# Performance work log

Hardware: AMD Instinct MI355X
Metric: run time of the kernel (lower is better)

## Reference

```python
import jax, jax.numpy as jnp
import numpy as np

EMBED_DIM = 1024
LATEN_DIM = 1024
B, S = 4, 2048


def setup_inputs() -> dict:
    key = jax.random.key(0)
    k1, k2, k3, k4, k5 = jax.random.split(key, 5)
    xq = jax.random.normal(k1, (B, S, EMBED_DIM), dtype=jnp.float32)
    xk = jax.random.normal(k2, (B, S, EMBED_DIM), dtype=jnp.float32)
    xv = jax.random.normal(k3, (B, S, EMBED_DIM), dtype=jnp.float32)
    # Linear weight init similar to torch default scale
    bound = 1.0 / np.sqrt(EMBED_DIM)
    Wq = jax.random.uniform(k4, (EMBED_DIM, EMBED_DIM), minval=-bound, maxval=bound, dtype=jnp.float32)
    bq = jax.random.uniform(k5, (EMBED_DIM,), minval=-bound, maxval=bound, dtype=jnp.float32)
    # causal mask: 1 => masked (future positions)
    att_mask = jnp.triu(jnp.ones((S, S), dtype=jnp.int32), k=1)
    return {"xq": xq, "xk": xk, "xv": xv, "Wq": Wq, "bq": bq, "att_mask": att_mask}


def reference(xq, xk, xv, Wq, bq, att_mask):
    scale = LATEN_DIM ** (-0.5)
    # Faithful to source: linearQ is applied to all three inputs.
    Q = jnp.einsum('bsd,ed->bse', xq, Wq) + bq
    K = jnp.einsum('bsd,ed->bse', xk, Wq) + bq
    V = jnp.einsum('bsd,ed->bse', xv, Wq) + bq
    scores = jnp.einsum('bqe,bke->bqk', Q, K) * scale  # [B, S, S]
    scores = jnp.where(att_mask == 1, -jnp.inf, scores)
    probs = jax.nn.softmax(scores, axis=-1)
    return jnp.einsum('bqk,bke->bqe', probs, V)
```

## Files before the change

kernel.cpp:

```cpp
#include <hip/hip_runtime.h>
#include <hip/hip_bf16.h>
#include <stdint.h>


typedef __attribute__((ext_vector_type(8))) short bf16x8;
typedef __attribute__((ext_vector_type(4))) float floatx4;

#define DEVI static __device__ __forceinline__

static constexpr int S_ = 2048;
static constexpr int E_ = 1024;
static constexpr int BATCH = 4;
static constexpr int N4X = 8192 * 1024 / 4;

DEVI unsigned short f2b(float f) {
  union { float f; unsigned u; } v; v.f = f;
  return (unsigned short)((v.u + 0x7FFFu + ((v.u >> 16) & 1u)) >> 16);
}

DEVI void async_load16(const void* g, void* l) {
  __builtin_amdgcn_global_load_lds(
      (__attribute__((address_space(1))) void*)(void*)(g),
      (__attribute__((address_space(3))) void*)(l),
      16, 0, 0);
}


DEVI void stage64(const unsigned short* __restrict__ src, unsigned short* ls,
                  int ld, int tid) {
#pragma unroll
  for (int j = 0; j < 4; ++j) {
    const int u = tid + j * 256;
    const int row = u >> 3, slot = u & 7;
    async_load16(src + (size_t)row * ld + ((slot ^ (row & 7)) << 3),
                 ls + u * 8);
  }
}

DEVI bf16x8 ldfrag64(const unsigned short* ls, int r, int c) {
  return *(const bf16x8*)(ls + r * 64 + ((c ^ (r & 7)) << 3));
}

DEVI void mfma_tile64(const unsigned short* lsA, const unsigned short* lsB,
                      int m0, int n0, int lrow, int g, floatx4 (&acc)[4][4]) {
#pragma unroll
  for (int ks = 0; ks < 2; ++ks) {
    bf16x8 af[4], bfr[4];
#pragma unroll
    for (int i = 0; i < 4; ++i)
      af[i] = ldfrag64(lsA, m0 + i * 16 + lrow, ks * 4 + g);
#pragma unroll
    for (int i = 0; i < 4; ++i)
      bfr[i] = ldfrag64(lsB, n0 + i * 16 + lrow, ks * 4 + g);
#pragma unroll
    for (int mi = 0; mi < 4; ++mi)
#pragma unroll
      for (int ni = 0; ni < 4; ++ni)
        acc[mi][ni] = __builtin_amdgcn_mfma_f32_16x16x32_bf16(
            af[mi], bfr[ni], acc[mi][ni], 0, 0, 0);
  }
}

__global__ void cvt_all(const float* __restrict__ xq,
                        const float* __restrict__ xk,
                        const float* __restrict__ xv,
                        const float* __restrict__ Wq,
                        unsigned short* __restrict__ Xb,
                        unsigned short* __restrict__ Wb) {
  int i = blockIdx.x * blockDim.x + threadIdx.x;
  const float4* src;
  ushort4* dst;
  if (i < 3 * N4X) {
    int seg = i / N4X, off = i - seg * N4X;
    const float* s = (seg == 0) ? xq : (seg == 1) ? xk : xv;
    src = (const float4*)s + off;
    dst = (ushort4*)(Xb + (size_t)seg * 8192 * 1024) + off;
  } else {
    int off = i - 3 * N4X;
    src = (const float4*)Wq + off;
    dst = (ushort4*)Wb + off;
  }
  float4 v = *src;
  ushort4 o;
  o.x = f2b(v.x); o.y = f2b(v.y); o.z = f2b(v.z); o.w = f2b(v.w);
  *dst = o;
}

__global__ __launch_bounds__(256) void gemm_qkv(
    const unsigned short* __restrict__ Xb, const unsigned short* __restrict__ Wb,
    const float* __restrict__ bias, unsigned short* __restrict__ Qb,
    unsigned short* __restrict__ Kb, unsigned short* __restrict__ Vt) {
  __shared__ __align__(16) unsigned short lsA[128 * 64];
  __shared__ __align__(16) unsigned short lsB[128 * 64];
  const int l = blockIdx.x;
  const int xcd = l & 7, i = l >> 3;
  const int bn = i & 7;
  const int bmg = xcd * 24 + (i >> 3);
  const int input = bmg / 64, bm = bmg % 64;
  const unsigned short* A = Xb + (size_t)bmg * 128 * 1024;
  const unsigned short* W = Wb + (size_t)bn * 128 * 1024;

  const int tid = threadIdx.x;
  const int lane = tid & 63, wave = tid >> 6;
  const int m0 = (wave >> 1) * 64, n0 = (wave & 1) * 64;
  const int lrow = lane & 15, g = lane >> 4;

  floatx4 acc[4][4] = {};
  for (int kt = 0; kt < 16; ++kt) {
    if (kt) __syncthreads();
    stage64(A + kt * 64, lsA, 1024, tid);
    stage64(W + kt * 64, lsB, 1024, tid);
    __syncthreads();
    mfma_tile64(lsA, lsB, m0, n0, lrow, g, acc);
  }

  unsigned short* C = (input == 0) ? Qb : (input == 1) ? Kb : Vt;
  const int rb = (lane >> 4) * 4;
#pragma unroll
  for (int mi = 0; mi < 4; ++mi)
#pragma unroll
    for (int ni = 0; ni < 4; ++ni) {
      int gcol = bn * 128 + n0 + ni * 16 + lrow;
      float bv = bias[gcol];
#pragma unroll
      for (int r = 0; r < 4; ++r) {
        int grow = bm * 128 + m0 + mi * 16 + rb + r;
        unsigned short val = f2b(acc[mi][ni][r] + bv);
        if (input == 2) {
          int b = grow >> 11, s = grow & 2047;
          C[((size_t)b * 1024 + gcol) * 2048 + s] = val;
        } else {
          C[(size_t)grow * 1024 + gcol] = val;
        }
      }
    }
}

__global__ __launch_bounds__(256) void gemm_scores_exp(
    const unsigned short* __restrict__ Qb,
    const unsigned short* __restrict__ Kb, unsigned short* __restrict__ P,
    float* __restrict__ lsum) {
  const int l = blockIdx.x;
  const int xcd = l & 7, k = l >> 3;
  const int m = k & 7, gl = k >> 3;
  const int gg = xcd * 12 + gl;
  const int z = gg / 24, r0 = gg % 24;
  const int bm = (r0 < 8) ? r0 : 8 + ((r0 - 8) >> 1);
  const int bn = ((r0 < 8) ? 0 : ((r0 - 8) & 1)) * 8 + m;
  if (bn > bm) return;

  __shared__ __align__(16) unsigned short lsA[128 * 64];
  __shared__ __align__(16) unsigned short lsB[128 * 64];
  const unsigned short* A = Qb + ((size_t)z * S_ + bm * 128) * E_;
  const unsigned short* Bt = Kb + ((size_t)z * S_ + bn * 128) * E_;
  const int tid = threadIdx.x;
  const int lane = tid & 63, wave = tid >> 6;
  const int m0 = (wave >> 1) * 64, n0 = (wave & 1) * 64;
  const int lrow = lane & 15, g = lane >> 4;

  floatx4 acc[4][4] = {};
  for (int kt = 0; kt < 16; ++kt) {
    if (kt) __syncthreads();
    stage64(A + kt * 64, lsA, E_, tid);
    stage64(Bt + kt * 64, lsB, E_, tid);
    __syncthreads();
    mfma_tile64(lsA, lsB, m0, n0, lrow, g, acc);
  }

  const int rb = (lane >> 4) * 4;
  const bool diag = (bm == bn);
#pragma unroll
  for (int mi = 0; mi < 4; ++mi)
#pragma unroll
    for (int r = 0; r < 4; ++r) {
      const int grow = bm * 128 + m0 + mi * 16 + rb + r;
      float rsum = 0.f;
#pragma unroll
      for (int ni = 0; ni < 4; ++ni) {
        const int gcol = bn * 128 + n0 + ni * 16 + lrow;
        float p = __expf(acc[mi][ni][r] * 0.03125f);
        if (diag && gcol > grow) p = 0.f;
        P[((size_t)z * S_ + grow) * S_ + gcol] = f2b(p);
        rsum += p;
      }
#pragma unroll
      for (int off = 1; off < 16; off <<= 1) rsum += __shfl_xor(rsum, off);
      if ((lane & 15) == 0) atomicAdd(&lsum[z * S_ + grow], rsum);
    }
}

__global__ __launch_bounds__(256) void gemm_pv(
    const unsigned short* __restrict__ Pb,
    const unsigned short* __restrict__ Vt, const float* __restrict__ lsum,
    float* __restrict__ Out) {
  __shared__ __align__(16) unsigned short lsA[128 * 64];
  __shared__ __align__(16) unsigned short lsB[128 * 64];
  const int l = blockIdx.x;
  const int xcd = l & 7, i = l >> 3;
  const int bn = i & 7, j = i >> 3;
  const int z = j >> 1;
  const int bm = (j & 1) ? xcd : 15 - xcd;

  const unsigned short* A = Pb + ((size_t)z * S_ + bm * 128) * S_;
  const unsigned short* Bt = Vt + ((size_t)z * E_ + bn * 128) * S_;
  float* C = Out + (size_t)z * S_ * E_;
  const int tid = threadIdx.x;
  const int lane = tid & 63, wave = tid >> 6;
  const int m0 = (wave >> 1) * 64, n0 = (wave & 1) * 64;
  const int lrow = lane & 15, g = lane >> 4;

  floatx4 acc[4][4] = {};
  const int nKK = (bm + 1) * 2;
  for (int kt = 0; kt < nKK; ++kt) {
    if (kt) __syncthreads();
    stage64(A + kt * 64, lsA, S_, tid);
    stage64(Bt + kt * 64, lsB, S_, tid);
    __syncthreads();
    mfma_tile64(lsA, lsB, m0, n0, lrow, g, acc);
  }

  const int rb = (lane >> 4) * 4;
#pragma unroll
  for (int mi = 0; mi < 4; ++mi)
#pragma unroll
    for (int r = 0; r < 4; ++r) {
      const int grow = bm * 128 + m0 + mi * 16 + rb + r;
      const float inv = 1.0f / lsum[z * S_ + grow];
#pragma unroll
      for (int ni = 0; ni < 4; ++ni) {
        const int gcol = bn * 128 + n0 + ni * 16 + lrow;
        C[(size_t)grow * E_ + gcol] = acc[mi][ni][r] * inv;
      }
    }
}

extern "C" void kernel_launch(void* const* d_in, const int* in_sizes, int n_in,
                              void* d_out, int out_size, void* d_ws,
                              size_t ws_size, hipStream_t stream) {
  (void)in_sizes; (void)n_in; (void)out_size; (void)ws_size;
  const float* xq = (const float*)d_in[0];
  const float* xk = (const float*)d_in[1];
  const float* xv = (const float*)d_in[2];
  const float* Wq = (const float*)d_in[3];
  const float* bq = (const float*)d_in[4];
  float* out = (float*)d_out;

  unsigned short* base16 = (unsigned short*)d_ws;
  unsigned short* Xb = base16;
  unsigned short* P = base16;
  unsigned short* Wb = base16 + (size_t)24 * 1024 * 1024;
  unsigned short* Qb = Wb + (size_t)1024 * 1024;
  unsigned short* Kb = Qb + (size_t)8192 * 1024;
  unsigned short* Vt = Kb + (size_t)8192 * 1024;
  float* lsum = (float*)(Vt + (size_t)8192 * 1024);

  hipMemsetAsync(lsum, 0, BATCH * S_ * sizeof(float), stream);

  const int n4tot = 3 * N4X + 1024 * 1024 / 4;
  cvt_all<<<n4tot / 256, 256, 0, stream>>>(xq, xk, xv, Wq, Xb, Wb);

  gemm_qkv<<<1536, 256, 0, stream>>>(Xb, Wb, bq, Qb, Kb, Vt);
  gemm_scores_exp<<<768, 256, 0, stream>>>(Qb, Kb, P, lsum);
  gemm_pv<<<512, 256, 0, stream>>>(P, Vt, lsum, out);
}
```

Before: 306.0 us.

## Use 64x128 tiles with 128-thread blocks for scores and PV GEMMs

The scores and PV kernels switch from 128x128 tiles on 256 threads to 64x128 tiles on 128 threads (two waves). The scores grid is rebuilt to enumerate only the causal lower-triangle tiles (1088 blocks, none exiting early), and PV uses 1024 blocks with a finer per-row-tile K range. This is meant to cut the masked work wasted above the diagonal and improve load balance across CUs. The cost is lower data reuse per tile, which means more global loads per FLOP.

```diff
diff --git a/kernel.cpp b/kernel.cpp
--- a/kernel.cpp
+++ b/kernel.cpp
@@ -26,11 +26,12 @@
 }
 
 
+template <int ROWS, int NTHR>
 DEVI void stage64(const unsigned short* __restrict__ src, unsigned short* ls,
                   int ld, int tid) {
 #pragma unroll
-  for (int j = 0; j < 4; ++j) {
-    const int u = tid + j * 256;
+  for (int j = 0; j < ROWS * 8 / NTHR; ++j) {
+    const int u = tid + j * NTHR;
     const int row = u >> 3, slot = u & 7;
     async_load16(src + (size_t)row * ld + ((slot ^ (row & 7)) << 3),
                  ls + u * 8);
@@ -108,8 +109,8 @@
   floatx4 acc[4][4] = {};
   for (int kt = 0; kt < 16; ++kt) {
     if (kt) __syncthreads();
-    stage64(A + kt * 64, lsA, 1024, tid);
-    stage64(W + kt * 64, lsB, 1024, tid);
+    stage64<128, 256>(A + kt * 64, lsA, 1024, tid);
+    stage64<128, 256>(W + kt * 64, lsB, 1024, tid);
     __syncthreads();
     mfma_tile64(lsA, lsB, m0, n0, lrow, g, acc);
   }
@@ -136,49 +137,48 @@
     }
 }
 
-__global__ __launch_bounds__(256) void gemm_scores_exp(
+__global__ __launch_bounds__(128) void gemm_scores_exp(
     const unsigned short* __restrict__ Qb,
     const unsigned short* __restrict__ Kb, unsigned short* __restrict__ P,
     float* __restrict__ lsum) {
+  __shared__ __align__(16) unsigned short lsA[64 * 64];
+  __shared__ __align__(16) unsigned short lsB[128 * 64];
   const int l = blockIdx.x;
-  const int xcd = l & 7, k = l >> 3;
-  const int m = k & 7, gl = k >> 3;
-  const int gg = xcd * 12 + gl;
-  const int z = gg / 24, r0 = gg % 24;
-  const int bm = (r0 < 8) ? r0 : 8 + ((r0 - 8) >> 1);
-  const int bn = ((r0 < 8) ? 0 : ((r0 - 8) & 1)) * 8 + m;
-  if (bn > bm) return;
-
-  __shared__ __align__(16) unsigned short lsA[128 * 64];
-  __shared__ __align__(16) unsigned short lsB[128 * 64];
-  const unsigned short* A = Qb + ((size_t)z * S_ + bm * 128) * E_;
-  const unsigned short* Bt = Kb + ((size_t)z * S_ + bn * 128) * E_;
+  const int gid = (l & 7) * 136 + (l >> 3);
+  const int z = gid >> 8 >= 0 ? gid / 272 : 0;
+  int r = gid % 272;
+  int rm = 0;
+  for (;;) { const int c = (rm >> 1) + 1; if (r < c) break; r -= c; ++rm; }
+  const int cn = r;
+
+  const unsigned short* A = Qb + ((size_t)z * S_ + rm * 64) * E_;
+  const unsigned short* Bt = Kb + ((size_t)z * S_ + cn * 128) * E_;
   const int tid = threadIdx.x;
   const int lane = tid & 63, wave = tid >> 6;
-  const int m0 = (wave >> 1) * 64, n0 = (wave & 1) * 64;
+  const int n0 = wave * 64;
   const int lrow = lane & 15, g = lane >> 4;
 
   floatx4 acc[4][4] = {};
   for (int kt = 0; kt < 16; ++kt) {
     if (kt) __syncthreads();
-    stage64(A + kt * 64, lsA, E_, tid);
-    stage64(Bt + kt * 64, lsB, E_, tid);
+    stage64<64, 128>(A + kt * 64, lsA, E_, tid);
+    stage64<128, 128>(Bt + kt * 64, lsB, E_, tid);
     __syncthreads();
-    mfma_tile64(lsA, lsB, m0, n0, lrow, g, acc);
+    mfma_tile64(lsA, lsB, 0, n0, lrow, g, acc);
   }
 
   const int rb = (lane >> 4) * 4;
-  const bool diag = (bm == bn);
+  const bool diag = (cn == (rm >> 1));
 #pragma unroll
   for (int mi = 0; mi < 4; ++mi)
 #pragma unroll
-    for (int r = 0; r < 4; ++r) {
-      const int grow = bm * 128 + m0 + mi * 16 + rb + r;
+    for (int r2 = 0; r2 < 4; ++r2) {
+      const int grow = rm * 64 + mi * 16 + rb + r2;
       float rsum = 0.f;
 #pragma unroll
       for (int ni = 0; ni < 4; ++ni) {
-        const int gcol = bn * 128 + n0 + ni * 16 + lrow;
-        float p = __expf(acc[mi][ni][r] * 0.03125f);
+        const int gcol = cn * 128 + n0 + ni * 16 + lrow;
+        float p = __expf(acc[mi][ni][r2] * 0.03125f);
         if (diag && gcol > grow) p = 0.f;
         P[((size_t)z * S_ + grow) * S_ + gcol] = f2b(p);
         rsum += p;
@@ -189,47 +189,47 @@
     }
 }
 
-__global__ __launch_bounds__(256) void gemm_pv(
+__global__ __launch_bounds__(128) void gemm_pv(
     const unsigned short* __restrict__ Pb,
     const unsigned short* __restrict__ Vt, const float* __restrict__ lsum,
     float* __restrict__ Out) {
-  __shared__ __align__(16) unsigned short lsA[128 * 64];
+  __shared__ __align__(16) unsigned short lsA[64 * 64];
   __shared__ __align__(16) unsigned short lsB[128 * 64];
   const int l = blockIdx.x;
   const int xcd = l & 7, i = l >> 3;
-  const int bn = i & 7, j = i >> 3;
-  const int z = j >> 1;
-  const int bm = (j & 1) ? xcd : 15 - xcd;
-
-  const unsigned short* A = Pb + ((size_t)z * S_ + bm * 128) * S_;
+  const int z = i >> 5, bn = (i >> 2) & 7, s = i & 3;
+  const int pm = (s & 1) ? xcd : 15 - xcd;
+  const int rm = 2 * pm + (s >> 1);
+
+  const unsigned short* A = Pb + ((size_t)z * S_ + rm * 64) * S_;
   const unsigned short* Bt = Vt + ((size_t)z * E_ + bn * 128) * S_;
   float* C = Out + (size_t)z * S_ * E_;
   const int tid = threadIdx.x;
   const int lane = tid & 63, wave = tid >> 6;
-  const int m0 = (wave >> 1) * 64, n0 = (wave & 1) * 64;
+  const int n0 = wave * 64;
   const int lrow = lane & 15, g = lane >> 4;
 
   floatx4 acc[4][4] = {};
-  const int nKK = (bm + 1) * 2;
-  for (int kt = 0; kt < nKK; ++kt) {
+  const int NT = ((rm >> 1) + 1) * 2;
+  for (int kt = 0; kt < NT; ++kt) {
     if (kt) __syncthreads();
-    stage64(A + kt * 64, lsA, S_, tid);
-    stage64(Bt + kt * 64, lsB, S_, tid);
+    stage64<64, 128>(A + kt * 64, lsA, S_, tid);
+    stage64<128, 128>(Bt + kt * 64, lsB, S_, tid);
     __syncthreads();
-    mfma_tile64(lsA, lsB, m0, n0, lrow, g, acc);
+    mfma_tile64(lsA, lsB, 0, n0, lrow, g, acc);
   }
 
   const int rb = (lane >> 4) * 4;
 #pragma unroll
   for (int mi = 0; mi < 4; ++mi)
 #pragma unroll
-    for (int r = 0; r < 4; ++r) {
-      const int grow = bm * 128 + m0 + mi * 16 + rb + r;
+    for (int r2 = 0; r2 < 4; ++r2) {
+      const int grow = rm * 64 + mi * 16 + rb + r2;
       const float inv = 1.0f / lsum[z * S_ + grow];
 #pragma unroll
       for (int ni = 0; ni < 4; ++ni) {
         const int gcol = bn * 128 + n0 + ni * 16 + lrow;
-        C[(size_t)grow * E_ + gcol] = acc[mi][ni][r] * inv;
+        C[(size_t)grow * E_ + gcol] = acc[mi][ni][r2] * inv;
       }
     }
 }
@@ -260,6 +260,6 @@
   cvt_all<<<n4tot / 256, 256, 0, stream>>>(xq, xk, xv, Wq, Xb, Wb);
 
   gemm_qkv<<<1536, 256, 0, stream>>>(Xb, Wb, bq, Qb, Kb, Vt);
-  gemm_scores_exp<<<768, 256, 0, stream>>>(Qb, Kb, P, lsum);
-  gemm_pv<<<512, 256, 0, stream>>>(P, Vt, lsum, out);
-}
+  gemm_scores_exp<<<1088, 128, 0, stream>>>(Qb, Kb, P, lsum);
+  gemm_pv<<<1024, 128, 0, stream>>>(P, Vt, lsum, out);
+}
```

New measurement: 311.1 us. Within noise of the previous version (+1.6%).

## Load attention GEMM fragments directly from global memory, bypassing LDS staging

Applied to the files above, without the earlier changes.

The scores and PV GEMMs stop staging tiles through LDS with barriers. Each wave now loads its MFMA fragments straight from global memory (relying on L2/cache) using a register double-buffered loop. This removes the LDS round trip and the __syncthreads, but each block re-reads data other waves also need and issues less coalesced global loads. The projection GEMM keeps LDS staging with a templated stage function.

```diff
diff --git a/kernel.cpp b/kernel.cpp
--- a/kernel.cpp
+++ b/kernel.cpp
@@ -26,11 +26,12 @@
 }
 
 
+template <int ROWS, int NTHR>
 DEVI void stage64(const unsigned short* __restrict__ src, unsigned short* ls,
                   int ld, int tid) {
 #pragma unroll
-  for (int j = 0; j < 4; ++j) {
-    const int u = tid + j * 256;
+  for (int j = 0; j < ROWS * 8 / NTHR; ++j) {
+    const int u = tid + j * NTHR;
     const int row = u >> 3, slot = u & 7;
     async_load16(src + (size_t)row * ld + ((slot ^ (row & 7)) << 3),
                  ls + u * 8);
@@ -58,6 +59,59 @@
       for (int ni = 0; ni < 4; ++ni)
         acc[mi][ni] = __builtin_amdgcn_mfma_f32_16x16x32_bf16(
             af[mi], bfr[ni], acc[mi][ni], 0, 0, 0);
+  }
+}
+
+
+DEVI void ld_frags(const unsigned short* (&pa)[4], const unsigned short* (&pb)[4],
+                   bf16x8 (&x0)[4], bf16x8 (&x1)[4], bf16x8 (&y0)[4],
+                   bf16x8 (&y1)[4]) {
+#pragma unroll
+  for (int i = 0; i < 4; ++i) {
+    x0[i] = *(const bf16x8*)(pa[i]);
+    x1[i] = *(const bf16x8*)(pa[i] + 32);
+    y0[i] = *(const bf16x8*)(pb[i]);
+    y1[i] = *(const bf16x8*)(pb[i] + 32);
+    pa[i] += 64;
+    pb[i] += 64;
+  }
+}
+
+DEVI void mfma32(const bf16x8 (&x0)[4], const bf16x8 (&x1)[4],
+                 const bf16x8 (&y0)[4], const bf16x8 (&y1)[4],
+                 floatx4 (&acc)[4][4]) {
+#pragma unroll
+  for (int mi = 0; mi < 4; ++mi)
+#pragma unroll
+    for (int ni = 0; ni < 4; ++ni)
+      acc[mi][ni] = __builtin_amdgcn_mfma_f32_16x16x32_bf16(
+          x0[mi], y0[ni], acc[mi][ni], 0, 0, 0);
+#pragma unroll
+  for (int mi = 0; mi < 4; ++mi)
+#pragma unroll
+    for (int ni = 0; ni < 4; ++ni)
+      acc[mi][ni] = __builtin_amdgcn_mfma_f32_16x16x32_bf16(
+          x1[mi], y1[ni], acc[mi][ni], 0, 0, 0);
+}
+
+DEVI void kloop_l2(const unsigned short* __restrict__ A, int lda,
+                   const unsigned short* __restrict__ Bt, int ldb, int NT,
+                   int m0, int n0, int lane, floatx4 (&acc)[4][4]) {
+  const int lrow = lane & 15, g = lane >> 4;
+  const unsigned short* pa[4];
+  const unsigned short* pb[4];
+#pragma unroll
+  for (int i = 0; i < 4; ++i) {
+    pa[i] = A + (size_t)(m0 + i * 16 + lrow) * lda + g * 8;
+    pb[i] = Bt + (size_t)(n0 + i * 16 + lrow) * ldb + g * 8;
+  }
+  bf16x8 a0[4], a1[4], b0[4], b1[4], c0[4], c1[4], d0[4], d1[4];
+  ld_frags(pa, pb, a0, a1, b0, b1);
+  for (int kt = 0; kt + 2 <= NT; kt += 2) {
+    ld_frags(pa, pb, c0, c1, d0, d1);
+    mfma32(a0, a1, b0, b1, acc);
+    if (kt + 2 < NT) ld_frags(pa, pb, a0, a1, b0, b1);
+    mfma32(c0, c1, d0, d1, acc);
   }
 }
 
@@ -108,8 +162,8 @@
   floatx4 acc[4][4] = {};
   for (int kt = 0; kt < 16; ++kt) {
     if (kt) __syncthreads();
-    stage64(A + kt * 64, lsA, 1024, tid);
-    stage64(W + kt * 64, lsB, 1024, tid);
+    stage64<128, 256>(A + kt * 64, lsA, 1024, tid);
+    stage64<128, 256>(W + kt * 64, lsB, 1024, tid);
     __syncthreads();
     mfma_tile64(lsA, lsB, m0, n0, lrow, g, acc);
   }
@@ -149,24 +203,16 @@
   const int bn = ((r0 < 8) ? 0 : ((r0 - 8) & 1)) * 8 + m;
   if (bn > bm) return;
 
-  __shared__ __align__(16) unsigned short lsA[128 * 64];
-  __shared__ __align__(16) unsigned short lsB[128 * 64];
   const unsigned short* A = Qb + ((size_t)z * S_ + bm * 128) * E_;
   const unsigned short* Bt = Kb + ((size_t)z * S_ + bn * 128) * E_;
   const int tid = threadIdx.x;
   const int lane = tid & 63, wave = tid >> 6;
   const int m0 = (wave >> 1) * 64, n0 = (wave & 1) * 64;
-  const int lrow = lane & 15, g = lane >> 4;
 
   floatx4 acc[4][4] = {};
-  for (int kt = 0; kt < 16; ++kt) {
-    if (kt) __syncthreads();
-    stage64(A + kt * 64, lsA, E_, tid);
-    stage64(Bt + kt * 64, lsB, E_, tid);
-    __syncthreads();
-    mfma_tile64(lsA, lsB, m0, n0, lrow, g, acc);
-  }
-
+  kloop_l2(A, E_, Bt, E_, 16, m0, n0, lane, acc);
+
+  const int lrow = lane & 15;
   const int rb = (lane >> 4) * 4;
   const bool diag = (bm == bn);
 #pragma unroll
@@ -193,8 +239,6 @@
     const unsigned short* __restrict__ Pb,
     const unsigned short* __restrict__ Vt, const float* __restrict__ lsum,
     float* __restrict__ Out) {
-  __shared__ __align__(16) unsigned short lsA[128 * 64];
-  __shared__ __align__(16) unsigned short lsB[128 * 64];
   const int l = blockIdx.x;
   const int xcd = l & 7, i = l >> 3;
   const int bn = i & 7, j = i >> 3;
@@ -207,18 +251,12 @@
   const int tid = threadIdx.x;
   const int lane = tid & 63, wave = tid >> 6;
   const int m0 = (wave >> 1) * 64, n0 = (wave & 1) * 64;
-  const int lrow = lane & 15, g = lane >> 4;
 
   floatx4 acc[4][4] = {};
-  const int nKK = (bm + 1) * 2;
-  for (int kt = 0; kt < nKK; ++kt) {
-    if (kt) __syncthreads();
-    stage64(A + kt * 64, lsA, S_, tid);
-    stage64(Bt + kt * 64, lsB, S_, tid);
-    __syncthreads();
-    mfma_tile64(lsA, lsB, m0, n0, lrow, g, acc);
-  }
-
+  const int NT = (bm + 1) * 2;
+  kloop_l2(A, S_, Bt, S_, NT, m0, n0, lane, acc);
+
+  const int lrow = lane & 15;
   const int rb = (lane >> 4) * 4;
 #pragma unroll
   for (int mi = 0; mi < 4; ++mi)
```

Result: slower. 433.2 us (+41.6%).

## Move V projection into scores kernel to fill idle tile slots

Applied to the files above, without the earlier changes.

The V projection GEMM is split out of the QKV kernel and appended as extra blocks (indices 768 and up) of the scores/exp kernel. The Q/K projection kernel now launches only 1024 blocks. The scores grid has many causally-skipped tiles that return immediately, so the V tiles can fill that spare capacity and run alongside the scores work instead of in their own stage. In exchange the fused kernel carries two code paths, and the V-transposed stores may compete with the P writes for memory bandwidth. stage64 is also templated on rows and thread count, with the same values used everywhere.

```diff
diff --git a/kernel.cpp b/kernel.cpp
--- a/kernel.cpp
+++ b/kernel.cpp
@@ -26,11 +26,12 @@
 }
 
 
+template <int ROWS, int NTHR>
 DEVI void stage64(const unsigned short* __restrict__ src, unsigned short* ls,
                   int ld, int tid) {
 #pragma unroll
-  for (int j = 0; j < 4; ++j) {
-    const int u = tid + j * 256;
+  for (int j = 0; j < ROWS * 8 / NTHR; ++j) {
+    const int u = tid + j * NTHR;
     const int row = u >> 3, slot = u & 7;
     async_load16(src + (size_t)row * ld + ((slot ^ (row & 7)) << 3),
                  ls + u * 8);
@@ -86,17 +87,17 @@
   *dst = o;
 }
 
-__global__ __launch_bounds__(256) void gemm_qkv(
+__global__ __launch_bounds__(256) void gemm_qk(
     const unsigned short* __restrict__ Xb, const unsigned short* __restrict__ Wb,
     const float* __restrict__ bias, unsigned short* __restrict__ Qb,
-    unsigned short* __restrict__ Kb, unsigned short* __restrict__ Vt) {
+    unsigned short* __restrict__ Kb) {
   __shared__ __align__(16) unsigned short lsA[128 * 64];
   __shared__ __align__(16) unsigned short lsB[128 * 64];
   const int l = blockIdx.x;
   const int xcd = l & 7, i = l >> 3;
   const int bn = i & 7;
-  const int bmg = xcd * 24 + (i >> 3);
-  const int input = bmg / 64, bm = bmg % 64;
+  const int bmg = xcd * 16 + (i >> 3);
+  const int input = bmg >> 6, bm = bmg & 63;
   const unsigned short* A = Xb + (size_t)bmg * 128 * 1024;
   const unsigned short* W = Wb + (size_t)bn * 128 * 1024;
 
@@ -108,13 +109,13 @@
   floatx4 acc[4][4] = {};
   for (int kt = 0; kt < 16; ++kt) {
     if (kt) __syncthreads();
-    stage64(A + kt * 64, lsA, 1024, tid);
-    stage64(W + kt * 64, lsB, 1024, tid);
+    stage64<128, 256>(A + kt * 64, lsA, 1024, tid);
+    stage64<128, 256>(W + kt * 64, lsB, 1024, tid);
     __syncthreads();
     mfma_tile64(lsA, lsB, m0, n0, lrow, g, acc);
   }
 
-  unsigned short* C = (input == 0) ? Qb : (input == 1) ? Kb : Vt;
+  unsigned short* C = input ? Kb : Qb;
   const int rb = (lane >> 4) * 4;
 #pragma unroll
   for (int mi = 0; mi < 4; ++mi)
@@ -125,68 +126,97 @@
 #pragma unroll
       for (int r = 0; r < 4; ++r) {
         int grow = bm * 128 + m0 + mi * 16 + rb + r;
-        unsigned short val = f2b(acc[mi][ni][r] + bv);
-        if (input == 2) {
-          int b = grow >> 11, s = grow & 2047;
-          C[((size_t)b * 1024 + gcol) * 2048 + s] = val;
-        } else {
-          C[(size_t)grow * 1024 + gcol] = val;
-        }
-      }
-    }
-}
-
-__global__ __launch_bounds__(256) void gemm_scores_exp(
+        C[(size_t)grow * 1024 + gcol] = f2b(acc[mi][ni][r] + bv);
+      }
+    }
+}
+
+__global__ __launch_bounds__(256) void gemm_scores_v(
+    const unsigned short* __restrict__ Xb,
+    const unsigned short* __restrict__ Wb, const float* __restrict__ bias,
     const unsigned short* __restrict__ Qb,
     const unsigned short* __restrict__ Kb, unsigned short* __restrict__ P,
-    float* __restrict__ lsum) {
-  const int l = blockIdx.x;
-  const int xcd = l & 7, k = l >> 3;
-  const int m = k & 7, gl = k >> 3;
-  const int gg = xcd * 12 + gl;
-  const int z = gg / 24, r0 = gg % 24;
-  const int bm = (r0 < 8) ? r0 : 8 + ((r0 - 8) >> 1);
-  const int bn = ((r0 < 8) ? 0 : ((r0 - 8) & 1)) * 8 + m;
-  if (bn > bm) return;
-
+    float* __restrict__ lsum, unsigned short* __restrict__ Vt) {
   __shared__ __align__(16) unsigned short lsA[128 * 64];
   __shared__ __align__(16) unsigned short lsB[128 * 64];
-  const unsigned short* A = Qb + ((size_t)z * S_ + bm * 128) * E_;
-  const unsigned short* Bt = Kb + ((size_t)z * S_ + bn * 128) * E_;
+  const int l = blockIdx.x;
   const int tid = threadIdx.x;
   const int lane = tid & 63, wave = tid >> 6;
   const int m0 = (wave >> 1) * 64, n0 = (wave & 1) * 64;
   const int lrow = lane & 15, g = lane >> 4;
-
-  floatx4 acc[4][4] = {};
-  for (int kt = 0; kt < 16; ++kt) {
-    if (kt) __syncthreads();
-    stage64(A + kt * 64, lsA, E_, tid);
-    stage64(Bt + kt * 64, lsB, E_, tid);
-    __syncthreads();
-    mfma_tile64(lsA, lsB, m0, n0, lrow, g, acc);
-  }
-
   const int rb = (lane >> 4) * 4;
-  const bool diag = (bm == bn);
-#pragma unroll
-  for (int mi = 0; mi < 4; ++mi)
-#pragma unroll
-    for (int r = 0; r < 4; ++r) {
-      const int grow = bm * 128 + m0 + mi * 16 + rb + r;
-      float rsum = 0.f;
+
+  if (l < 768) {
+    const int xcd = l & 7, k = l >> 3;
+    const int m = k & 7, gl = k >> 3;
+    const int gg = xcd * 12 + gl;
+    const int z = gg / 24, r0 = gg % 24;
+    const int bm = (r0 < 8) ? r0 : 8 + ((r0 - 8) >> 1);
+    const int bn = ((r0 < 8) ? 0 : ((r0 - 8) & 1)) * 8 + m;
+    if (bn > bm) return;
+
+    const unsigned short* A = Qb + ((size_t)z * S_ + bm * 128) * E_;
+    const unsigned short* Bt = Kb + ((size_t)z * S_ + bn * 128) * E_;
+
+    floatx4 acc[4][4] = {};
+    for (int kt = 0; kt < 16; ++kt) {
+      if (kt) __syncthreads();
+      stage64<128, 256>(A + kt * 64, lsA, E_, tid);
+      stage64<128, 256>(Bt + kt * 64, lsB, E_, tid);
+      __syncthreads();
+      mfma_tile64(lsA, lsB, m0, n0, lrow, g, acc);
+    }
+
+    const bool diag = (bm == bn);
+#pragma unroll
+    for (int mi = 0; mi < 4; ++mi)
+#pragma unroll
+      for (int r = 0; r < 4; ++r) {
+        const int grow = bm * 128 + m0 + mi * 16 + rb + r;
+        float rsum = 0.f;
+#pragma unroll
+        for (int ni = 0; ni < 4; ++ni) {
+          const int gcol = bn * 128 + n0 + ni * 16 + lrow;
+          float p = __expf(acc[mi][ni][r] * 0.03125f);
+          if (diag && gcol > grow) p = 0.f;
+          P[((size_t)z * S_ + grow) * S_ + gcol] = f2b(p);
+          rsum += p;
+        }
+#pragma unroll
+        for (int off = 1; off < 16; off <<= 1) rsum += __shfl_xor(rsum, off);
+        if ((lane & 15) == 0) atomicAdd(&lsum[z * S_ + grow], rsum);
+      }
+  } else {
+    const int lv = l - 768;
+    const int xcd = lv & 7, i = lv >> 3;
+    const int bn = i & 7;
+    const int bm = xcd * 8 + (i >> 3);
+    const unsigned short* A = Xb + (size_t)(128 + bm) * 128 * 1024;
+    const unsigned short* W = Wb + (size_t)bn * 128 * 1024;
+
+    floatx4 acc[4][4] = {};
+    for (int kt = 0; kt < 16; ++kt) {
+      if (kt) __syncthreads();
+      stage64<128, 256>(A + kt * 64, lsA, 1024, tid);
+      stage64<128, 256>(W + kt * 64, lsB, 1024, tid);
+      __syncthreads();
+      mfma_tile64(lsA, lsB, m0, n0, lrow, g, acc);
+    }
+
+#pragma unroll
+    for (int mi = 0; mi < 4; ++mi)
 #pragma unroll
       for (int ni = 0; ni < 4; ++ni) {
-        const int gcol = bn * 128 + n0 + ni * 16 + lrow;
-        float p = __expf(acc[mi][ni][r] * 0.03125f);
-        if (diag && gcol > grow) p = 0.f;
-        P[((size_t)z * S_ + grow) * S_ + gcol] = f2b(p);
-        rsum += p;
-      }
-#pragma unroll
-      for (int off = 1; off < 16; off <<= 1) rsum += __shfl_xor(rsum, off);
-      if ((lane & 15) == 0) atomicAdd(&lsum[z * S_ + grow], rsum);
-    }
+        int gcol = bn * 128 + n0 + ni * 16 + lrow;
+        float bv = bias[gcol];
+#pragma unroll
+        for (int r = 0; r < 4; ++r) {
+          int grow = bm * 128 + m0 + mi * 16 + rb + r;
+          int b = grow >> 11, s = grow & 2047;
+          Vt[((size_t)b * 1024 + gcol) * 2048 + s] = f2b(acc[mi][ni][r] + bv);
+        }
+      }
+  }
 }
 
 __global__ __launch_bounds__(256) void gemm_pv(
@@ -213,8 +243,8 @@
   const int nKK = (bm + 1) * 2;
   for (int kt = 0; kt < nKK; ++kt) {
     if (kt) __syncthreads();
-    stage64(A + kt * 64, lsA, S_, tid);
-    stage64(Bt + kt * 64, lsB, S_, tid);
+    stage64<128, 256>(A + kt * 64, lsA, S_, tid);
+    stage64<128, 256>(Bt + kt * 64, lsB, S_, tid);
     __syncthreads();
     mfma_tile64(lsA, lsB, m0, n0, lrow, g, acc);
   }
@@ -259,7 +289,7 @@
   const int n4tot = 3 * N4X + 1024 * 1024 / 4;
   cvt_all<<<n4tot / 256, 256, 0, stream>>>(xq, xk, xv, Wq, Xb, Wb);
 
-  gemm_qkv<<<1536, 256, 0, stream>>>(Xb, Wb, bq, Qb, Kb, Vt);
-  gemm_scores_exp<<<768, 256, 0, stream>>>(Qb, Kb, P, lsum);
+  gemm_qk<<<1024, 256, 0, stream>>>(Xb, Wb, bq, Qb, Kb);
+  gemm_scores_v<<<1280, 256, 0, stream>>>(Xb, Wb, bq, Qb, Kb, P, lsum, Vt);
   gemm_pv<<<512, 256, 0, stream>>>(P, Vt, lsum, out);
 }
```

New measurement: 278.3 us. 9.1% less time.
